# Optimization experiments

Hardware: AMD Instinct MI355X
Metric: run time of the kernel (lower is better)

## Reference

```python
import jax, jax.numpy as jnp
import numpy as np

N_EMBD = 1024
N_HEAD = 16


def setup_inputs() -> dict:
    key = jax.random.key(0)
    ks = jax.random.split(key, 5)
    B, T, C = 2, 2048, N_EMBD
    x = jax.random.normal(ks[0], (B, T, C), dtype=jnp.float32)
    # parameters (stored as (in, out); forward uses x @ W + b, equivalent to torch Linear)
    s1 = 1.0 / np.sqrt(C)
    W_attn = jax.random.normal(ks[1], (C, 3 * C), dtype=jnp.float32) * s1
    b_attn = jnp.zeros((3 * C,), dtype=jnp.float32)
    W_proj = jax.random.normal(ks[2], (C, C), dtype=jnp.float32) * s1
    b_proj = jnp.zeros((C,), dtype=jnp.float32)
    return {"x": x, "W_attn": W_attn, "b_attn": b_attn, "W_proj": W_proj, "b_proj": b_proj}


def reference(x, W_attn, b_attn, W_proj, b_proj):
    B, T, C = x.shape
    H = N_HEAD
    D = C // H  # head dim
    qkv = x @ W_attn + b_attn                       # [B, T, 3C]
    q, k, v = jnp.split(qkv, 3, axis=-1)
    # [B, H, T, D]
    q = q.reshape(B, T, H, D).transpose(0, 2, 1, 3)
    k = k.reshape(B, T, H, D).transpose(0, 2, 1, 3)
    v = v.reshape(B, T, H, D).transpose(0, 2, 1, 3)
    scale = 1.0 / jnp.sqrt(jnp.asarray(D, dtype=q.dtype))
    wei = jnp.einsum("bhqd,bhkd->bhqk", q, k) * scale  # [B, H, T, T]
    causal = jnp.tril(jnp.ones((T, T), dtype=bool))
    wei = jnp.where(causal[None, None, :, :], wei, -jnp.inf)
    wei = jax.nn.softmax(wei, axis=-1)
    y = jnp.einsum("bhqk,bhkd->bhqd", wei, v)          # [B, H, T, D]
    y = y.transpose(0, 2, 1, 3).reshape(B, T, C)
    return y @ W_proj + b_proj
```

## Files before the change

### kernel.cpp

```cpp
#include <hip/hip_runtime.h>
#include <hip/hip_bf16.h>

typedef __attribute__((ext_vector_type(8))) short short8;
typedef __attribute__((ext_vector_type(4))) float floatx4;
typedef __attribute__((ext_vector_type(4))) unsigned int uintx4;
#define BF16 __hip_bfloat16

__device__ __forceinline__ unsigned short f2bf(float f) {
  unsigned int u = __builtin_bit_cast(unsigned int, f);
  unsigned int r = (u + 0x7FFFu + ((u >> 16) & 1u)) >> 16;
  return (unsigned short)r;
}

__device__ __forceinline__ unsigned int cvt_pk_bf16(float lo, float hi) {
  unsigned int r;
  asm("v_cvt_pk_bf16_f32 %0, %1, %2" : "=v"(r) : "v"(lo), "v"(hi));
  return r;
}

__device__ __forceinline__ void gload_lds16(const void* g, void* l) {
  __builtin_amdgcn_global_load_lds(
      (const __attribute__((address_space(1))) unsigned int*)g,
      (__attribute__((address_space(3))) unsigned int*)l, 16, 0, 0);
}

__global__ __launch_bounds__(256)
void cvt_bf16(const float* __restrict__ in, unsigned short* __restrict__ out, int n) {
  int i = (blockIdx.x * 256 + threadIdx.x) * 8;
  if (i >= n) return;
  float4 a = *(const float4*)(in + i);
  float4 b = *(const float4*)(in + i + 4);
  short8 v;
  v[0] = (short)f2bf(a.x); v[1] = (short)f2bf(a.y);
  v[2] = (short)f2bf(a.z); v[3] = (short)f2bf(a.w);
  v[4] = (short)f2bf(b.x); v[5] = (short)f2bf(b.y);
  v[6] = (short)f2bf(b.z); v[7] = (short)f2bf(b.w);
  *(short8*)(out + i) = v;
}

__global__ __launch_bounds__(256)
void transpose_cvt(const float* __restrict__ in, unsigned short* __restrict__ out,
                   int K, int N) {
  __shared__ float tile[64][65];
  const int nb = N >> 6;
  const int tn = blockIdx.x % nb, tk = blockIdx.x / nb;
  const int n0 = tn << 6, k0 = tk << 6;
  const int tid = threadIdx.x;
#pragma unroll
  for (int c = 0; c < 4; ++c) {
    int t = tid + c * 256;
    int r = t >> 4, col = (t & 15) << 2;
    float4 v = *(const float4*)(in + (size_t)(k0 + r) * N + n0 + col);
    tile[r][col] = v.x; tile[r][col + 1] = v.y;
    tile[r][col + 2] = v.z; tile[r][col + 3] = v.w;
  }
  __syncthreads();
#pragma unroll
  for (int c = 0; c < 2; ++c) {
    int t = tid + c * 256;
    int r = t >> 3, col = (t & 7) << 3;
    short8 v;
#pragma unroll
    for (int j = 0; j < 8; ++j) v[j] = (short)f2bf(tile[col + j][r]);
    *(short8*)(out + (size_t)(n0 + r) * K + k0 + col) = v;
  }
}

__global__ __launch_bounds__(512, 4)
void gemm_qkv(const BF16* __restrict__ A, const BF16* __restrict__ Bt,
              const float* __restrict__ bias, BF16* __restrict__ out,
              int M, int N, int K) {
  const int tid = threadIdx.x;
  const int w = tid >> 6, l = tid & 63;
  const int lr = l & 15, lg = l >> 4;
  const int bm = blockIdx.x >> 4, bn = blockIdx.x & 15;
  const int row0 = bm << 7;
  const int col0 = bn * 192;
  const int wr = (w >> 2) << 6;
  const int wc = (w & 3) * 48;

  __shared__ __align__(16) BF16 ldsA[2][128 * 64];
  __shared__ __align__(16) BF16 ldsB[2][192 * 64];

  floatx4 acc[4][3] = {};
  const int swzl = (lr & 7) << 3;

#define QSTAGE(K0, BUF)                                                       \
  {                                                                           \
    _Pragma("unroll")                                                         \
    for (int c = 0; c < 2; ++c) {                  \
      int t = w * 64 + l + c * 512;                                           \
      int ar = t >> 3;                                                        \
      int ch = (t & 7) ^ (ar & 7);                                            \
      gload_lds16(A + (size_t)(row0 + ar) * K + (K0) + (ch << 3),             \
                  &ldsA[BUF][w * 512 + c * 4096]);                            \
    }                                                                         \
    _Pragma("unroll")                                                         \
    for (int c = 0; c < 3; ++c) {                  \
      int t = w * 64 + l + c * 512;                                           \
      int br = t >> 3;                                                        \
      int ch = (t & 7) ^ (br & 7);                                            \
      gload_lds16(Bt + (size_t)(col0 + br) * K + (K0) + (ch << 3),            \
                  &ldsB[BUF][w * 512 + c * 4096]);                            \
    }                                                                         \
  }

  const int NT = K >> 6;
  QSTAGE(0, 0);

  for (int kt = 0; kt < NT; ++kt) {
    const int cur = kt & 1;
    if (kt + 1 < NT) {
      QSTAGE((kt + 1) << 6, cur ^ 1);
      asm volatile("s_waitcnt vmcnt(5)" ::: "memory");
    } else {
      asm volatile("s_waitcnt vmcnt(0)" ::: "memory");
    }
    __builtin_amdgcn_s_barrier();

#pragma unroll
    for (int kk = 0; kk < 64; kk += 32) {
      short8 af[4], bf[3];
#pragma unroll
      for (int m = 0; m < 4; ++m)
        af[m] = *(const short8*)(&ldsA[cur][(wr + m * 16 + lr) * 64 + ((kk + lg * 8) ^ swzl)]);
#pragma unroll
      for (int n = 0; n < 3; ++n)
        bf[n] = *(const short8*)(&ldsB[cur][(wc + n * 16 + lr) * 64 + ((kk + lg * 8) ^ swzl)]);
#pragma unroll
      for (int m = 0; m < 4; ++m)
#pragma unroll
        for (int n = 0; n < 3; ++n)
          acc[m][n] = __builtin_amdgcn_mfma_f32_16x16x32_bf16(af[m], bf[n], acc[m][n], 0, 0, 0);
    }
    if (kt + 1 < NT) __builtin_amdgcn_s_barrier();
  }
#undef QSTAGE

#pragma unroll
  for (int m = 0; m < 4; ++m)
#pragma unroll
    for (int n = 0; n < 3; ++n)
#pragma unroll
      for (int j = 0; j < 4; ++j) {
        int row = row0 + wr + m * 16 + lg * 4 + j;
        int col = col0 + wc + n * 16 + lr;
        float v = acc[m][n][j] + bias[col];
        int s = col >> 10, cc = col & 1023;
        int hh = cc >> 6, dd = cc & 63;
        int bb = row >> 11, tt = row & 2047;
        size_t addr;
        if (s == 2)
          addr = (size_t)8388608 + (((size_t)bb * 16 + hh) * 64 + dd) * 2048 + tt;
        else
          addr = (size_t)s * 4194304 + (((size_t)bb * 16 + hh) * 2048 + tt) * 64 + dd;
        out[addr] = __float2bfloat16(v);
      }
}

__global__ __launch_bounds__(256, 2)
void gemm_proj(const BF16* __restrict__ A, const BF16* __restrict__ Bt,
               const float* __restrict__ bias, float* __restrict__ out,
               int M, int N, int K) {
  const int tid = threadIdx.x;
  const int w = tid >> 6, l = tid & 63;
  const int lr = l & 15, lg = l >> 4;
  const int nbx = N >> 7;
  const int bm = blockIdx.x / nbx, bn = blockIdx.x % nbx;
  const int row0 = bm << 7, col0 = bn << 7;
  const int wr = (w >> 1) << 6, wc = (w & 1) << 6;

  __shared__ __align__(16) BF16 ldsA[128 * 64];
  __shared__ __align__(16) BF16 ldsB[128 * 64];

  floatx4 acc[4][4] = {};
  const int swzl = (lr & 7) << 3;

  for (int k0 = 0; k0 < K; k0 += 64) {
#pragma unroll
    for (int c = 0; c < 4; ++c) {
      int t = w * 64 + l + c * 256;
      int ar = t >> 3;
      int ch = (t & 7) ^ (ar & 7);
      gload_lds16(A + (size_t)(row0 + ar) * K + k0 + (ch << 3),
                  ldsA + w * 512 + c * 2048);
      gload_lds16(Bt + (size_t)(col0 + ar) * K + k0 + (ch << 3),
                  ldsB + w * 512 + c * 2048);
    }
    __syncthreads();
#pragma unroll
    for (int kk = 0; kk < 64; kk += 32) {
      short8 af[4], bf[4];
#pragma unroll
      for (int m = 0; m < 4; ++m)
        af[m] = *(const short8*)(ldsA + (wr + m * 16 + lr) * 64 + ((kk + lg * 8) ^ swzl));
#pragma unroll
      for (int n = 0; n < 4; ++n)
        bf[n] = *(const short8*)(ldsB + (wc + n * 16 + lr) * 64 + ((kk + lg * 8) ^ swzl));
#pragma unroll
      for (int m = 0; m < 4; ++m)
#pragma unroll
        for (int n = 0; n < 4; ++n)
          acc[m][n] = __builtin_amdgcn_mfma_f32_16x16x32_bf16(af[m], bf[n], acc[m][n], 0, 0, 0);
    }
    __syncthreads();
  }

#pragma unroll
  for (int m = 0; m < 4; ++m)
#pragma unroll
    for (int n = 0; n < 4; ++n)
#pragma unroll
      for (int j = 0; j < 4; ++j) {
        int row = row0 + wr + m * 16 + lg * 4 + j;
        int col = col0 + wc + n * 16 + lr;
        out[(size_t)row * N + col] = acc[m][n][j] + bias[col];
      }
}

__global__ __launch_bounds__(256, 5)
void flash_attn(const BF16* __restrict__ qkv, float* __restrict__ PO,
                float* __restrict__ PL) {
  const int T = 2048;
  const int bid = blockIdx.x;
  const int J = bid >> 5;
  const int bh = bid & 31;
  const int qt = 31 - (J >> 1);
  const int par = J & 1;
  const int q0 = qt << 6;
  const int n = qt + 1;
  const int iters = (n - par + 1) >> 1;
  const int tid = threadIdx.x, w = tid >> 6, l = tid & 63;
  const int lr = l & 15, lg = l >> 4;

  const BF16* Q  = qkv + (size_t)bh * (T * 64);
  const BF16* Kp = qkv + 4194304 + (size_t)bh * (T * 64);
  const BF16* Vt = qkv + 8388608 + (size_t)bh * (64 * T);

  __shared__ __align__(16) BF16 ldsK[2][4096];
  __shared__ __align__(16) BF16 ldsV[2][4096];

  const float C1 = 0.18033688011112042f;
  const float C2 = 17.312340490667562f;
  const int swzl = (lr & 7) << 3;

  short8 qf[2];
#pragma unroll
  for (int c = 0; c < 2; ++c)
    qf[c] = *(const short8*)(Q + (size_t)(q0 + w * 16 + lr) * 64 + c * 32 + lg * 8);

  floatx4 acc_o[4] = {};
  floatx4 lsum4 = {0.f, 0.f, 0.f, 0.f};

  const int t0 = w * 64 + l, t1 = t0 + 256;
  const int r0 = t0 >> 3, ch0 = (t0 & 7) ^ (r0 & 7);
  const int r1 = t1 >> 3, ch1 = (t1 & 7) ^ (r1 & 7);
  const BF16* kg0 = Kp + (((size_t)(par * 64 + r0)) << 6) + ch0 * 8;
  const BF16* kg1 = Kp + (((size_t)(par * 64 + r1)) << 6) + ch1 * 8;
  const BF16* vg0 = Vt + (size_t)r0 * T + par * 64 + ch0 * 8;
  const BF16* vg1 = Vt + (size_t)r1 * T + par * 64 + ch1 * 8;

#define STAGE2(BUF)                                           \
  {                                                           \
    gload_lds16(kg0, &ldsK[BUF][w * 512]);                    \
    gload_lds16(vg0, &ldsV[BUF][w * 512]);                    \
    gload_lds16(kg1, &ldsK[BUF][w * 512 + 2048]);             \
    gload_lds16(vg1, &ldsV[BUF][w * 512 + 2048]);             \
    kg0 += 8192; kg1 += 8192; vg0 += 128; vg1 += 128;         \
  }

#define TILE(IT, MASKED)                                                      \
  {                                                                           \
    const int cur_ = (IT) & 1;                                                \
    if ((IT) + 1 < iters) {                                                   \
      STAGE2(cur_ ^ 1);                                                       \
      asm volatile("s_waitcnt vmcnt(4)" ::: "memory");                        \
    } else {                                                                  \
      asm volatile("s_waitcnt vmcnt(0)" ::: "memory");                        \
    }                                                                         \
    __builtin_amdgcn_s_barrier();                                             \
    floatx4 accs[4] = {};                                                     \
    __builtin_amdgcn_s_setprio(1);                                            \
    _Pragma("unroll")                                                         \
    for (int c = 0; c < 2; ++c)                                               \
      _Pragma("unroll")                                                       \
      for (int n4 = 0; n4 < 4; ++n4) {                                        \
        short8 kf = *(const short8*)(&ldsK[cur_][(n4 * 16 + lr) * 64 +        \
                                                ((c * 32 + lg * 8) ^ swzl)]); \
        accs[n4] = __builtin_amdgcn_mfma_f32_16x16x32_bf16(kf, qf[c], accs[n4], 0, 0, 0); \
      }                                                                       \
    __builtin_amdgcn_s_setprio(0);                                            \
    _Pragma("unroll")                                                         \
    for (int n4 = 0; n4 < 4; ++n4)                                            \
      _Pragma("unroll")                                                       \
      for (int j = 0; j < 4; ++j) {                                           \
        float p = exp2f(fmaf(accs[n4][j], C1, -C2));                          \
        if (MASKED && (n4 * 16 + lg * 4 + j > w * 16 + lr)) p = 0.f;          \
        lsum4[j] += p;                                                        \
        accs[n4][j] = p;                                                      \
      }                                                                       \
    __builtin_amdgcn_s_setprio(1);                                            \
    _Pragma("unroll")                                                         \
    for (int c = 0; c < 2; ++c) {                                             \
      unsigned int a0 = cvt_pk_bf16(accs[2 * c][0], accs[2 * c][1]);          \
      unsigned int b0 = cvt_pk_bf16(accs[2 * c + 1][0], accs[2 * c + 1][1]);  \
      unsigned int a1 = cvt_pk_bf16(accs[2 * c][2], accs[2 * c][3]);          \
      unsigned int b1 = cvt_pk_bf16(accs[2 * c + 1][2], accs[2 * c + 1][3]);  \
      asm("v_permlane32_swap_b32 %0, %1" : "+v"(a0), "+v"(b0));               \
      asm("v_permlane32_swap_b32 %0, %1" : "+v"(a1), "+v"(b1));               \
      asm("v_permlane16_swap_b32 %0, %1" : "+v"(a0), "+v"(b0));               \
      asm("v_permlane16_swap_b32 %0, %1" : "+v"(a1), "+v"(b1));               \
      uintx4 pw; pw[0] = a0; pw[1] = a1; pw[2] = b0; pw[3] = b1;              \
      short8 pf = __builtin_bit_cast(short8, pw);                             \
      _Pragma("unroll")                                                       \
      for (int n4 = 0; n4 < 4; ++n4) {                                        \
        short8 vf = *(const short8*)(&ldsV[cur_][(n4 * 16 + lr) * 64 +        \
                                                ((c * 32 + lg * 8) ^ swzl)]); \
        acc_o[n4] = __builtin_amdgcn_mfma_f32_16x16x32_bf16(pf, vf, acc_o[n4], 0, 0, 0); \
      }                                                                       \
    }                                                                         \
    __builtin_amdgcn_s_setprio(0);                                            \
    __builtin_amdgcn_s_barrier();                                             \
  }

  const int full = iters - ((par == (qt & 1)) ? 1 : 0);
  if (iters > 0) {
    STAGE2(0);
    for (int it = 0; it < full; ++it) TILE(it, false);
    if (full < iters) TILE(full, true);
  }
#undef TILE
#undef STAGE2

  const int slot = (bh * 32 + qt) * 2 + par;
  float lsum = (lsum4[0] + lsum4[1]) + (lsum4[2] + lsum4[3]);
  lsum += __shfl_xor(lsum, 16, 64);
  lsum += __shfl_xor(lsum, 32, 64);
  if (lg == 0) PL[slot * 64 + w * 16 + lr] = lsum;
  float* po = PO + (size_t)slot * 4096;
#pragma unroll
  for (int n4 = 0; n4 < 4; ++n4)
#pragma unroll
    for (int j = 0; j < 4; ++j)
      po[(w * 16 + lg * 4 + j) * 64 + n4 * 16 + lr] = acc_o[n4][j];
}

__global__ __launch_bounds__(256)
void attn_merge(const float* __restrict__ PO, const float* __restrict__ PL,
                BF16* __restrict__ y) {
  const int g = blockIdx.x * 256 + threadIdx.x;
  const int qi = g >> 9;
  const int rem = (g & 511) << 3;
  const int r = rem >> 6, d0 = rem & 63;
  const float* A = PO + (size_t)qi * 8192 + rem;
  const float* B = A + 4096;
  const float lA = PL[qi * 128 + r];
  const float lB = PL[qi * 128 + 64 + r];
  const float inv = 1.0f / (lA + lB);
  float4 a0 = *(const float4*)A, a1 = *(const float4*)(A + 4);
  float4 b0 = *(const float4*)B, b1 = *(const float4*)(B + 4);
  const int bh = qi >> 5, qt = qi & 31;
  const int b = bh >> 4, h = bh & 15;
  const int t = qt * 64 + r;
  short8 v;
  v[0] = (short)f2bf((a0.x + b0.x) * inv);
  v[1] = (short)f2bf((a0.y + b0.y) * inv);
  v[2] = (short)f2bf((a0.z + b0.z) * inv);
  v[3] = (short)f2bf((a0.w + b0.w) * inv);
  v[4] = (short)f2bf((a1.x + b1.x) * inv);
  v[5] = (short)f2bf((a1.y + b1.y) * inv);
  v[6] = (short)f2bf((a1.z + b1.z) * inv);
  v[7] = (short)f2bf((a1.w + b1.w) * inv);
  *(short8*)(y + ((size_t)b * 2048 + t) * 1024 + h * 64 + d0) = v;
}

extern "C" void kernel_launch(void* const* d_in, const int* in_sizes, int n_in,
                              void* d_out, int out_size, void* d_ws, size_t ws_size,
                              hipStream_t stream) {
  const float* x      = (const float*)d_in[0];
  const float* W_attn = (const float*)d_in[1];
  const float* b_attn = (const float*)d_in[2];
  const float* W_proj = (const float*)d_in[3];
  const float* b_proj = (const float*)d_in[4];
  float* out = (float*)d_out;
  BF16* ws  = (BF16*)d_ws;

  BF16* xb      = ws;
  BF16* wt_attn = xb + 4194304;
  BF16* wt_proj = wt_attn + 3145728;
  BF16* qkv     = wt_proj + 1048576;
  BF16* y       = qkv + 12582912;
  float* PO     = (float*)(y + 4194304);
  float* PL     = PO + 8388608;

  hipLaunchKernelGGL(cvt_bf16, dim3(2048), dim3(256), 0, stream,
                     x, (unsigned short*)xb, 4194304);
  hipLaunchKernelGGL(transpose_cvt, dim3(48 * 16), dim3(256), 0, stream,
                     W_attn, (unsigned short*)wt_attn, 1024, 3072);
  hipLaunchKernelGGL(transpose_cvt, dim3(16 * 16), dim3(256), 0, stream,
                     W_proj, (unsigned short*)wt_proj, 1024, 1024);
  hipLaunchKernelGGL(gemm_qkv, dim3(512), dim3(512), 0, stream,
                     xb, wt_attn, b_attn, qkv, 4096, 3072, 1024);
  hipLaunchKernelGGL(flash_attn, dim3(2048), dim3(256), 0, stream, qkv, PO, PL);
  hipLaunchKernelGGL(attn_merge, dim3(2048), dim3(256), 0, stream, PO, PL, y);
  hipLaunchKernelGGL(gemm_proj, dim3(32 * 8), dim3(256), 0, stream,
                     y, wt_proj, b_proj, out, 4096, 1024, 1024);
}
```

Before: 124.5 us.

## Restructure QKV GEMM into 256x192 tiles with phased load/MFMA interleave

The QKV projection GEMM now uses 256x192 block tiles with 8x3 accumulators per wave and half as many blocks. Each k-step is split into four phases that interleave LDS fragment reads, prefetches of the next tile into LDS, and MFMA groups, using sched_barrier, s_setprio and explicit barriers. A block-id remap groups blocks that share operands so they run close together. The aim is to raise arithmetic intensity and hide global load latency behind MFMA work, at the cost of more registers and LDS per block (occupancy bound drops from 4 to 2) and 256 blocks on a GPU with 256 CUs.

```diff
diff --git a/kernel.cpp b/kernel.cpp
--- a/kernel.cpp
+++ b/kernel.cpp
@@ -66,85 +66,137 @@
   }
 }
 
-__global__ __launch_bounds__(512, 4)
+__global__ __launch_bounds__(512, 2)
 void gemm_qkv(const BF16* __restrict__ A, const BF16* __restrict__ Bt,
               const float* __restrict__ bias, BF16* __restrict__ out,
               int M, int N, int K) {
   const int tid = threadIdx.x;
   const int w = tid >> 6, l = tid & 63;
   const int lr = l & 15, lg = l >> 4;
-  const int bm = blockIdx.x >> 4, bn = blockIdx.x & 15;
-  const int row0 = bm << 7;
+  const int bid = (int)blockIdx.x;
+  const int bidp = (bid & 7) * 32 + (bid >> 3);
+  const int bm = bidp & 15, bn = bidp >> 4;
+  const int row0 = bm << 8;
   const int col0 = bn * 192;
-  const int wr = (w >> 2) << 6;
-  const int wc = (w & 3) * 48;
-
-  __shared__ __align__(16) BF16 ldsA[2][128 * 64];
+  const int wm = w >> 2, wn = w & 3;
+  const int r0 = wm << 7;
+  const int c0w = wn * 48;
+
+  __shared__ __align__(16) BF16 ldsA[2][256 * 64];
   __shared__ __align__(16) BF16 ldsB[2][192 * 64];
 
-  floatx4 acc[4][3] = {};
+  floatx4 acc[8][3] = {};
   const int swzl = (lr & 7) << 3;
 
-#define QSTAGE(K0, BUF)                                                       \
-  {                                                                           \
-    _Pragma("unroll")                                                         \
-    for (int c = 0; c < 2; ++c) {                  \
-      int t = w * 64 + l + c * 512;                                           \
-      int ar = t >> 3;                                                        \
-      int ch = (t & 7) ^ (ar & 7);                                            \
-      gload_lds16(A + (size_t)(row0 + ar) * K + (K0) + (ch << 3),             \
-                  &ldsA[BUF][w * 512 + c * 4096]);                            \
-    }                                                                         \
-    _Pragma("unroll")                                                         \
-    for (int c = 0; c < 3; ++c) {                  \
-      int t = w * 64 + l + c * 512;                                           \
-      int br = t >> 3;                                                        \
-      int ch = (t & 7) ^ (br & 7);                                            \
-      gload_lds16(Bt + (size_t)(col0 + br) * K + (K0) + (ch << 3),            \
-                  &ldsB[BUF][w * 512 + c * 4096]);                            \
-    }                                                                         \
-  }
+#define STAGE_A(K0, DST, c)                                                   \
+  { int t_ = tid + (c) * 512; int ar_ = t_ >> 3;                              \
+    int ch_ = (t_ & 7) ^ (ar_ & 7);                                           \
+    gload_lds16(A + (size_t)(row0 + ar_) * K + (K0) + (ch_ << 3),             \
+                (DST) + w * 512 + (c) * 4096); }
+#define STAGE_B(K0, DST, c)                                                   \
+  { int t_ = tid + (c) * 512; int br_ = t_ >> 3;                              \
+    int ch_ = (t_ & 7) ^ (br_ & 7);                                           \
+    gload_lds16(Bt + (size_t)(col0 + br_) * K + (K0) + (ch_ << 3),            \
+                (DST) + w * 512 + (c) * 4096); }
+
+#define PH_PRE                                                                \
+  __builtin_amdgcn_sched_barrier(0);                                          \
+  __builtin_amdgcn_s_barrier();                                               \
+  asm volatile("s_waitcnt lgkmcnt(0)" ::: "memory");                          \
+  __builtin_amdgcn_sched_barrier(0);                                          \
+  __builtin_amdgcn_s_setprio(1);
+#define PH_POST                                                               \
+  __builtin_amdgcn_s_setprio(0);                                              \
+  __builtin_amdgcn_s_barrier();                                               \
+  __builtin_amdgcn_sched_barrier(0);
+
+  STAGE_A(0, &ldsA[0][0], 0); STAGE_A(0, &ldsA[0][0], 1);
+  STAGE_A(0, &ldsA[0][0], 2); STAGE_A(0, &ldsA[0][0], 3);
+  STAGE_B(0, &ldsB[0][0], 0); STAGE_B(0, &ldsB[0][0], 1);
+  STAGE_B(0, &ldsB[0][0], 2);
+  asm volatile("s_waitcnt vmcnt(0)" ::: "memory");
+  __builtin_amdgcn_s_barrier();
 
   const int NT = K >> 6;
-  QSTAGE(0, 0);
-
-  for (int kt = 0; kt < NT; ++kt) {
-    const int cur = kt & 1;
-    if (kt + 1 < NT) {
-      QSTAGE((kt + 1) << 6, cur ^ 1);
-      asm volatile("s_waitcnt vmcnt(5)" ::: "memory");
-    } else {
-      asm volatile("s_waitcnt vmcnt(0)" ::: "memory");
-    }
+  for (int t = 0; t < NT; ++t) {
+    const int cur = t & 1;
+    const BF16* cA = &ldsA[cur][0];
+    const BF16* cB = &ldsB[cur][0];
+    BF16* nA = &ldsA[cur ^ 1][0];
+    BF16* nB = &ldsB[cur ^ 1][0];
+    const int kn = (t + 1) << 6;
+    const bool hn = (t + 1) < NT;
+
+#define LDA(row, kk) (*(const short8*)(cA + (row) * 64 + (((kk) + lg * 8) ^ swzl)))
+#define LDB(row, kk) (*(const short8*)(cB + (row) * 64 + (((kk) + lg * 8) ^ swzl)))
+
+    short8 af[4], bf[3];
+
+#pragma unroll
+    for (int m = 0; m < 4; ++m) af[m] = LDA(r0 + m * 16 + lr, 0);
+#pragma unroll
+    for (int n = 0; n < 3; ++n) bf[n] = LDB(c0w + n * 16 + lr, 0);
+    if (hn) { STAGE_A(kn, nA, 0); STAGE_A(kn, nA, 1); STAGE_B(kn, nB, 0); }
+    PH_PRE
+#pragma unroll
+    for (int m = 0; m < 4; ++m)
+#pragma unroll
+      for (int n = 0; n < 3; ++n)
+        acc[m][n] = __builtin_amdgcn_mfma_f32_16x16x32_bf16(af[m], bf[n], acc[m][n], 0, 0, 0);
+    PH_POST
+
+#pragma unroll
+    for (int m = 0; m < 4; ++m) af[m] = LDA(r0 + 64 + m * 16 + lr, 0);
+    if (hn) { STAGE_A(kn, nA, 2); STAGE_A(kn, nA, 3); STAGE_B(kn, nB, 1); }
+    PH_PRE
+#pragma unroll
+    for (int m = 0; m < 4; ++m)
+#pragma unroll
+      for (int n = 0; n < 3; ++n)
+        acc[4 + m][n] = __builtin_amdgcn_mfma_f32_16x16x32_bf16(af[m], bf[n], acc[4 + m][n], 0, 0, 0);
+    PH_POST
+
+#pragma unroll
+    for (int m = 0; m < 4; ++m) af[m] = LDA(r0 + m * 16 + lr, 32);
+#pragma unroll
+    for (int n = 0; n < 3; ++n) bf[n] = LDB(c0w + n * 16 + lr, 32);
+    if (hn) { STAGE_B(kn, nB, 2); }
+    PH_PRE
+#pragma unroll
+    for (int m = 0; m < 4; ++m)
+#pragma unroll
+      for (int n = 0; n < 3; ++n)
+        acc[m][n] = __builtin_amdgcn_mfma_f32_16x16x32_bf16(af[m], bf[n], acc[m][n], 0, 0, 0);
+    PH_POST
+
+#pragma unroll
+    for (int m = 0; m < 4; ++m) af[m] = LDA(r0 + 64 + m * 16 + lr, 32);
+    PH_PRE
+#pragma unroll
+    for (int m = 0; m < 4; ++m)
+#pragma unroll
+      for (int n = 0; n < 3; ++n)
+        acc[4 + m][n] = __builtin_amdgcn_mfma_f32_16x16x32_bf16(af[m], bf[n], acc[4 + m][n], 0, 0, 0);
+    __builtin_amdgcn_s_setprio(0);
+    asm volatile("s_waitcnt vmcnt(0)" ::: "memory");
     __builtin_amdgcn_s_barrier();
-
-#pragma unroll
-    for (int kk = 0; kk < 64; kk += 32) {
-      short8 af[4], bf[3];
-#pragma unroll
-      for (int m = 0; m < 4; ++m)
-        af[m] = *(const short8*)(&ldsA[cur][(wr + m * 16 + lr) * 64 + ((kk + lg * 8) ^ swzl)]);
-#pragma unroll
-      for (int n = 0; n < 3; ++n)
-        bf[n] = *(const short8*)(&ldsB[cur][(wc + n * 16 + lr) * 64 + ((kk + lg * 8) ^ swzl)]);
-#pragma unroll
-      for (int m = 0; m < 4; ++m)
-#pragma unroll
-        for (int n = 0; n < 3; ++n)
-          acc[m][n] = __builtin_amdgcn_mfma_f32_16x16x32_bf16(af[m], bf[n], acc[m][n], 0, 0, 0);
-    }
-    if (kt + 1 < NT) __builtin_amdgcn_s_barrier();
-  }
-#undef QSTAGE
-
-#pragma unroll
-  for (int m = 0; m < 4; ++m)
+    __builtin_amdgcn_sched_barrier(0);
+#undef LDA
+#undef LDB
+  }
+#undef STAGE_A
+#undef STAGE_B
+#undef PH_PRE
+#undef PH_POST
+
+#pragma unroll
+  for (int m = 0; m < 8; ++m)
 #pragma unroll
     for (int n = 0; n < 3; ++n)
 #pragma unroll
       for (int j = 0; j < 4; ++j) {
-        int row = row0 + wr + m * 16 + lg * 4 + j;
-        int col = col0 + wc + n * 16 + lr;
+        int row = row0 + r0 + m * 16 + lg * 4 + j;
+        int col = col0 + c0w + n * 16 + lr;
         float v = acc[m][n][j] + bias[col];
         int s = col >> 10, cc = col & 1023;
         int hh = cc >> 6, dd = cc & 63;
@@ -399,7 +451,7 @@
                      W_attn, (unsigned short*)wt_attn, 1024, 3072);
   hipLaunchKernelGGL(transpose_cvt, dim3(16 * 16), dim3(256), 0, stream,
                      W_proj, (unsigned short*)wt_proj, 1024, 1024);
-  hipLaunchKernelGGL(gemm_qkv, dim3(512), dim3(512), 0, stream,
+  hipLaunchKernelGGL(gemm_qkv, dim3(256), dim3(512), 0, stream,
                      xb, wt_attn, b_attn, qkv, 4096, 3072, 1024);
   hipLaunchKernelGGL(flash_attn, dim3(2048), dim3(256), 0, stream, qkv, PO, PL);
   hipLaunchKernelGGL(attn_merge, dim3(2048), dim3(256), 0, stream, PO, PL, y);
```

Result: slower. 127.2 us (+2.2%).
